# Kernel tuning notes

Measured on AMD Instinct MI355X. Metric: run time of the kernel, lower is better.

## Reference

```python
import jax, jax.numpy as jnp
import numpy as np

D_MODEL = 256
MLP_DIM = 1024
EPS = 1e-5

def _layernorm(x, g, b):
    mu = jnp.mean(x, axis=-1, keepdims=True)
    var = jnp.mean(jnp.square(x - mu), axis=-1, keepdims=True)
    return (x - mu) * jax.lax.rsqrt(var + EPS) * g + b

def setup_inputs() -> dict:
    key = jax.random.key(0)
    ks = jax.random.split(key, 4)
    d, m = D_MODEL, MLP_DIM
    x = jax.random.normal(ks[0], (8, 1024, 4, d), dtype=jnp.float32)
    w_qkv = jax.random.normal(ks[1], (3 * d, d), dtype=jnp.float32) * 0.05  # torch Linear weight (out,in)
    gamma1 = jnp.ones((d,), jnp.float32)
    beta1 = jnp.zeros((d,), jnp.float32)
    gamma2 = jnp.ones((d,), jnp.float32)
    beta2 = jnp.zeros((d,), jnp.float32)
    w1 = jax.random.normal(ks[2], (m, d), dtype=jnp.float32) * 0.05
    b1 = jnp.zeros((m,), jnp.float32)
    w2 = jax.random.normal(ks[3], (d, m), dtype=jnp.float32) * 0.05
    b2 = jnp.zeros((d,), jnp.float32)
    return {"x": x, "w_qkv": w_qkv, "gamma1": gamma1, "beta1": beta1,
            "gamma2": gamma2, "beta2": beta2, "w1": w1, "b1": b1, "w2": w2, "b2": b2}

def reference(x, w_qkv, gamma1, beta1, gamma2, beta2, w1, b1, w2, b2):
    bsz, n, h, d = x.shape
    scale = d ** -0.5
    # --- attention branch: x + attn(norm1(x)) ---
    xn = _layernorm(x, gamma1, beta1)
    # Linear(d, 3d): xn @ W^T, then reshape trailing 3d -> (d, 3) as in torch
    qkv = jnp.einsum('bnhd,ed->bnhe', xn, w_qkv).reshape(bsz, n * h, d, 3)
    q, k, v = qkv[..., 0], qkv[..., 1], qkv[..., 2]   # [b, n*h, d]
    dots = jnp.einsum('bid,bjd->bij', q, k) * scale   # [b, n*h, n*h]
    attn = jax.nn.softmax(dots, axis=-1)              # dropout=0 -> identity
    out = jnp.einsum('bij,bjd->bid', attn, v).reshape(bsz, n, h, d)
    x = x + out
    # --- mlp branch: x + mlp(norm2(x)) ---
    xn2 = _layernorm(x, gamma2, beta2)
    hid = jax.nn.silu(jnp.einsum('bnhd,md->bnhm', xn2, w1) + b1)
    x = x + jnp.einsum('bnhm,dm->bnhd', hid, w2) + b2
    return x
```

## Files before the change

### kernel.cpp

```cpp
#include <hip/hip_runtime.h>


typedef __attribute__((ext_vector_type(8))) short bf16x8;
typedef __attribute__((ext_vector_type(4))) short bf16x4;
typedef __attribute__((ext_vector_type(4))) float f32x4;
typedef __attribute__((ext_vector_type(16))) float f32x16;

static __device__ __forceinline__ short f2bf(float f) {
    union { float f; unsigned u; } v; v.f = f;
    unsigned r = (v.u + 0x7FFFu + ((v.u >> 16) & 1u)) >> 16;
    return (short)r;
}

static __device__ __forceinline__ void gll16(const void* g, void* l) {
    __builtin_amdgcn_global_load_lds(
        (const __attribute__((address_space(1))) unsigned*)g,
        (__attribute__((address_space(3))) unsigned*)l, 16, 0, 0);
}

__global__ __launch_bounds__(256) void k_cvt(const float* __restrict__ wqkv,
                                             const float* __restrict__ w1,
                                             const float* __restrict__ w2,
                                             short* __restrict__ owqkv,
                                             short* __restrict__ ow1,
                                             short* __restrict__ ow2) {
    int i = blockIdx.x * 256 + threadIdx.x;
    if (i < 196608) {
        int e = i >> 8, col = i & 255;
        int dd = e / 3, which = e - dd * 3;
        float v = wqkv[i];
        if (which == 0) v *= 0.0625f * 1.44269504f;
        owqkv[((which << 8) + dd) * 256 + col] = f2bf(v);
    }
    if (i < 262144) { ow1[i] = f2bf(w1[i]); ow2[i] = f2bf(w2[i]); }
}

__global__ __launch_bounds__(256) void k_ln(const float* __restrict__ x,
                                            const float* __restrict__ g,
                                            const float* __restrict__ bta,
                                            short* __restrict__ out) {
    int w = threadIdx.x >> 6, lane = threadIdx.x & 63;
    long row = (long)blockIdx.x * 4 + w;
    float4 v = *((const float4*)(x + row * 256) + lane);
    float s = v.x + v.y + v.z + v.w;
    float q = v.x * v.x + v.y * v.y + v.z * v.z + v.w * v.w;
    for (int off = 1; off < 64; off <<= 1) {
        s += __shfl_xor(s, off);
        q += __shfl_xor(q, off);
    }
    float mean = s * (1.0f / 256.0f);
    float var = q * (1.0f / 256.0f) - mean * mean;
    float rstd = rsqrtf(var + 1e-5f);
    float4 gg = *((const float4*)g + lane);
    float4 bb = *((const float4*)bta + lane);
    short4 o;
    o.x = f2bf((v.x - mean) * rstd * gg.x + bb.x);
    o.y = f2bf((v.y - mean) * rstd * gg.y + bb.y);
    o.z = f2bf((v.z - mean) * rstd * gg.z + bb.z);
    o.w = f2bf((v.w - mean) * rstd * gg.w + bb.w);
    *((short4*)(out + row * 256) + lane) = o;
}

__global__ __launch_bounds__(256) void k_qkv(const short* __restrict__ xn,
                                             const short* __restrict__ wb,
                                             short* __restrict__ Q,
                                             short* __restrict__ K,
                                             short* __restrict__ VT) {
    __shared__ __attribute__((aligned(16))) short lds_a[64 * 256];
    __shared__ __attribute__((aligned(16))) short lds_b[64 * 256];
    int t = threadIdx.x, w = t >> 6, l = t & 63, l5 = l & 31;
    int m0 = blockIdx.y * 64, n0 = blockIdx.x * 64;
    const char* ga = (const char*)xn + (long)m0 * 512;
    const char* gb = (const char*)wb + (long)n0 * 512;
    #pragma unroll
    for (int i = 0; i < 8; i++) {
        int r = w * 16 + i * 2 + (l >> 5);
        int off = r * 512 + ((l5 ^ (r & 31)) * 16);
        int ldst = (w * 16 + i * 2) * 512;
        gll16(ga + off, (char*)lds_a + ldst);
        gll16(gb + off, (char*)lds_b + ldst);
    }
    __syncthreads();
    int ln = l & 15, qd = l >> 4;
    int moff = (w >> 1) * 32, noff = (w & 1) * 32;
    f32x4 acc[2][2] = {};
    #pragma unroll
    for (int ks = 0; ks < 8; ks++) {
        int ca = ks * 4 + qd;
        int ra0 = moff + ln, ra1 = moff + 16 + ln;
        int rb0 = noff + ln, rb1 = noff + 16 + ln;
        bf16x8 a0 = *(const bf16x8*)((const char*)lds_a + ra0 * 512 + ((ca ^ (ra0 & 31)) * 16));
        bf16x8 a1 = *(const bf16x8*)((const char*)lds_a + ra1 * 512 + ((ca ^ (ra1 & 31)) * 16));
        bf16x8 b0 = *(const bf16x8*)((const char*)lds_b + rb0 * 512 + ((ca ^ (rb0 & 31)) * 16));
        bf16x8 b1 = *(const bf16x8*)((const char*)lds_b + rb1 * 512 + ((ca ^ (rb1 & 31)) * 16));
        acc[0][0] = __builtin_amdgcn_mfma_f32_16x16x32_bf16(a0, b0, acc[0][0], 0, 0, 0);
        acc[0][1] = __builtin_amdgcn_mfma_f32_16x16x32_bf16(a0, b1, acc[0][1], 0, 0, 0);
        acc[1][0] = __builtin_amdgcn_mfma_f32_16x16x32_bf16(a1, b0, acc[1][0], 0, 0, 0);
        acc[1][1] = __builtin_amdgcn_mfma_f32_16x16x32_bf16(a1, b1, acc[1][1], 0, 0, 0);
    }
    if (blockIdx.x < 8) {
        #pragma unroll
        for (int mi = 0; mi < 2; mi++)
            #pragma unroll
            for (int nj = 0; nj < 2; nj++)
                #pragma unroll
                for (int rg = 0; rg < 4; rg++) {
                    int gr = m0 + moff + mi * 16 + qd * 4 + rg;
                    int e = n0 + noff + nj * 16 + ln;
                    short bv = f2bf(acc[mi][nj][rg]);
                    if (e < 256) Q[(long)gr * 256 + e] = bv;
                    else K[(long)gr * 256 + (e - 256)] = bv;
                }
    } else {
        __syncthreads();
        short* scr = lds_a;
        #pragma unroll
        for (int mi = 0; mi < 2; mi++)
            #pragma unroll
            for (int nj = 0; nj < 2; nj++)
                #pragma unroll
                for (int rg = 0; rg < 4; rg++) {
                    int dl = noff + nj * 16 + ln;
                    int il = moff + mi * 16 + qd * 4 + rg;
                    scr[dl * 88 + il] = f2bf(acc[mi][nj][rg]);
                }
        __syncthreads();
        int bb = m0 >> 12, i0 = m0 & 4095;
        int dl = t >> 2, ch = t & 3;
        const int4* s4 = (const int4*)(scr + dl * 88 + ch * 16);
        int4 v0 = s4[0], v1 = s4[1];
        long vrow = ((long)(bb * 256 + (n0 - 512) + dl)) * 4096 + i0 + ch * 16;
        *(int4*)(VT + vrow) = v0;
        *(int4*)(VT + vrow + 8) = v1;
    }
}

__global__ __launch_bounds__(512, 2) void k_attn(const short* __restrict__ Q,
                                                 const short* __restrict__ K,
                                                 const short* __restrict__ VT,
                                                 const float* __restrict__ x,
                                                 float* __restrict__ out) {
    __shared__ __attribute__((aligned(16))) short lds_k[2][64 * 256];
    __shared__ __attribute__((aligned(16))) short lds_v[2][2][256 * 40];
    int t = threadIdx.x, w = t >> 6, l = t & 63, l5 = l & 31, h = l >> 5;
    int ww = w & 3, hkv = w >> 2;
    int b = blockIdx.x;
    int q0 = blockIdx.y * 128 + ww * 32;

    bf16x8 qf[16];
    {
        const short* qrow = Q + ((long)(b * 4096 + q0 + l5)) * 256;
        #pragma unroll
        for (int kc = 0; kc < 16; kc++) qf[kc] = *(const bf16x8*)(qrow + kc * 16 + h * 8);
    }
    f32x16 O[8] = {};
    float lsum = 0.f;

    const char* Kb = (const char*)(K + (long)b * 4096 * 256);
    const int4* gv = (const int4*)(VT + (long)b * 4096 * 256);

    int koff[4], klds[4];
    #pragma unroll
    for (int i = 0; i < 4; i++) {
        int r = w * 8 + i * 2 + (l >> 5);
        koff[i] = r * 512 + ((l5 ^ (r & 31)) * 16);
        klds[i] = (w * 8 + i * 2) * 512;
    }
    int vgbase[4], vloff[4];
    #pragma unroll
    for (int i = 0; i < 4; i++) {
        int c = t + 512 * i;
        int sub = c >> 10, cc = c & 1023, d = cc >> 2, ch = cc & 3;
        vgbase[i] = d * 512 + sub * 4 + ch;
        vloff[i] = sub * 20480 + d * 80 + ch * 16;
    }
    int4 vs[4];

    #pragma unroll
    for (int i = 0; i < 4; i++) vs[i] = gv[vgbase[i]];
    #pragma unroll
    for (int i = 0; i < 4; i++) gll16(Kb + koff[i], (char*)lds_k[0] + klds[i]);
    #pragma unroll
    for (int i = 0; i < 4; i++)
        *(int4*)((char*)lds_v + vloff[i]) = vs[i];
    __syncthreads();

    const char* lvmine = (const char*)lds_v + hkv * 20480;

    for (int jt = 0; jt < 64; jt++) {
        int cur = jt & 1;
        if (jt < 63) {
            #pragma unroll
            for (int i = 0; i < 4; i++) vs[i] = gv[vgbase[i] + (jt + 1) * 8];
            int ka = (jt + 1) * 32768;
            #pragma unroll
            for (int i = 0; i < 4; i++)
                gll16(Kb + ka + koff[i], (char*)lds_k[cur ^ 1] + klds[i]);
        }
        const short* lk = lds_k[cur] + hkv * 32 * 256;
        const char* lv = lvmine + cur * 40960;
        f32x16 st = {};
        #pragma unroll
        for (int kc = 0; kc < 16; kc++) {
            int cc = kc * 2 + h;
            bf16x8 a = *(const bf16x8*)(lk + (l5 * 32 + (cc ^ l5)) * 8);
            st = __builtin_amdgcn_mfma_f32_32x32x16_bf16(a, qf[kc], st, 0, 0, 0);
        }
        unsigned pw[4][2];
        #pragma unroll
        for (int r4 = 0; r4 < 4; r4++) {
            float p0 = __builtin_amdgcn_exp2f(st[r4 * 4 + 0]);
            float p1 = __builtin_amdgcn_exp2f(st[r4 * 4 + 1]);
            float p2 = __builtin_amdgcn_exp2f(st[r4 * 4 + 2]);
            float p3 = __builtin_amdgcn_exp2f(st[r4 * 4 + 3]);
            lsum += (p0 + p1) + (p2 + p3);
            union { float f; unsigned u; } u0, u1, u2, u3;
            u0.f = p0; u1.f = p1; u2.f = p2; u3.f = p3;
            pw[r4][0] = __builtin_amdgcn_perm(u1.u + 0x8000u, u0.u + 0x8000u, 0x07060302u);
            pw[r4][1] = __builtin_amdgcn_perm(u3.u + 0x8000u, u2.u + 0x8000u, 0x07060302u);
        }
        bf16x8 pfr[2];
        #pragma unroll
        for (int k2 = 0; k2 < 2; k2++) {
            unsigned a0 = pw[2 * k2][0], a1 = pw[2 * k2][1];
            unsigned b0 = pw[2 * k2 + 1][0], b1 = pw[2 * k2 + 1][1];
            asm("v_permlane32_swap_b32 %0, %1" : "+v"(a0), "+v"(b0));
            asm("v_permlane32_swap_b32 %0, %1" : "+v"(a1), "+v"(b1));
            union { unsigned u[4]; bf16x8 v; } f;
            f.u[0] = a0; f.u[1] = a1; f.u[2] = b0; f.u[3] = b1;
            pfr[k2] = f.v;
        }
        if (jt < 63) {
            #pragma unroll
            for (int i = 0; i < 4; i++)
                *(int4*)((char*)lds_v + (cur ^ 1) * 40960 + vloff[i]) = vs[i];
        }
        #pragma unroll
        for (int dt = 0; dt < 8; dt++) {
            const char* vbase = lv + (dt * 32 + l5) * 80;
            #pragma unroll
            for (int k2 = 0; k2 < 2; k2++) {
                bf16x8 va = *(const bf16x8*)(vbase + (k2 * 2 + h) * 16);
                O[dt] = __builtin_amdgcn_mfma_f32_32x32x16_bf16(va, pfr[k2], O[dt], 0, 0, 0);
            }
        }
        __syncthreads();
    }

    float lt = lsum + __shfl_xor(lsum, 32);
    float* lmrg = (float*)&lds_v[1][0][0];
    lmrg[hkv * 128 + ww * 32 + l5] = lt;
    __syncthreads();
    float ltot = lmrg[ww * 32 + l5] + lmrg[128 + ww * 32 + l5];
    float rinv = 1.0f / ltot;

    float* omrg = (float*)&lds_v[0][0][0];
    float* fscr = (float*)lds_k[0] + ww * (32 * 33);
    #pragma unroll
    for (int dt = 0; dt < 8; dt++) {
        if (hkv == 1) {
            #pragma unroll
            for (int r = 0; r < 16; r++) omrg[ww * 1024 + r * 64 + l] = O[dt][r];
        }
        __syncthreads();
        if (hkv == 0) {
            #pragma unroll
            for (int r = 0; r < 16; r++) {
                float Om = O[dt][r] + omrg[ww * 1024 + r * 64 + l];
                int drow = (r & 3) + 8 * (r >> 2) + 4 * h;
                fscr[drow * 33 + l5] = Om * rinv;
            }
            asm volatile("s_waitcnt lgkmcnt(0)" ::: "memory");
            #pragma unroll
            for (int it = 0; it < 16; it++) {
                int ql = it * 2 + h;
                float v = fscr[l5 * 33 + ql];
                long idx = ((long)(b * 4096 + q0 + ql)) * 256 + dt * 32 + l5;
                out[idx] = x[idx] + v;
            }
            asm volatile("s_waitcnt lgkmcnt(0)" ::: "memory");
        }
        __syncthreads();
    }
}

__global__ __launch_bounds__(512, 2) void k_mlp(const short* __restrict__ xn,
                                                const short* __restrict__ w1b,
                                                const short* __restrict__ w2b,
                                                const float* __restrict__ b1,
                                                const float* __restrict__ b2,
                                                float* __restrict__ out) {
    __shared__ __attribute__((aligned(16))) short lds_w[2][32 * 256];
    __shared__ __attribute__((aligned(16))) short lds_h[8][16 * 264];
    int t = threadIdx.x, w = t >> 6, l = t & 63, l5 = l & 31, ln = l & 15, qd = l >> 4;
    int R0 = blockIdx.x * 128 + w * 16;
    short* lhs = lds_h[w];

    bf16x8 a1f[8];
    #pragma unroll
    for (int kc = 0; kc < 8; kc++)
        a1f[kc] = *(const bf16x8*)(xn + (long)(R0 + ln) * 256 + kc * 32 + qd * 8);

    long s1off[2], s2off[2]; int wlds[2];
    #pragma unroll
    for (int i = 0; i < 2; i++) {
        int r = w * 4 + i * 2 + (l >> 5);
        int ch = l5 ^ (r & 31);
        s1off[i] = (long)r * 512 + ch * 16;
        s2off[i] = (long)r * 2048 + ch * 16;
        wlds[i] = (w * 4 + i * 2) * 512;
    }
    const char* W1c = (const char*)w1b;
    const char* W2c = (const char*)w2b;

    f32x4 Oc[8][2] = {};
    #pragma unroll
    for (int i = 0; i < 2; i++)
        gll16(W1c + s1off[i], (char*)lds_w[0] + wlds[i]);
    __syncthreads();
    int cur = 0;

    for (int pass = 0; pass < 4; pass++) {
        #pragma unroll
        for (int nt = 0; nt < 8; nt++) {
            if (nt < 7) {
                long base = (long)(pass * 256 + (nt + 1) * 32) * 512;
                #pragma unroll
                for (int i = 0; i < 2; i++)
                    gll16(W1c + base + s1off[i], (char*)lds_w[cur ^ 1] + wlds[i]);
            } else {
                long base = (long)pass * 512;
                #pragma unroll
                for (int i = 0; i < 2; i++)
                    gll16(W2c + base + s2off[i], (char*)lds_w[cur ^ 1] + wlds[i]);
            }
            const short* lw = lds_w[cur];
            #pragma unroll
            for (int g = 0; g < 2; g++) {
                int lr = g * 16 + ln;
                f32x4 acc = {};
                #pragma unroll
                for (int kc = 0; kc < 8; kc++) {
                    int cc = kc * 4 + qd;
                    bf16x8 bf = *(const bf16x8*)(lw + lr * 256 + (cc ^ lr) * 8);
                    acc = __builtin_amdgcn_mfma_f32_16x16x32_bf16(a1f[kc], bf, acc, 0, 0, 0);
                }
                float bb = b1[pass * 256 + nt * 32 + lr];
                #pragma unroll
                for (int rg = 0; rg < 4; rg++) {
                    float z = acc[rg] + bb;
                    float sv = z / (1.0f + __expf(-z));
                    lhs[(qd * 4 + rg) * 264 + nt * 32 + lr] = f2bf(sv);
                }
            }
            __syncthreads();
            cur ^= 1;
        }
        bf16x8 a2f[8];
        #pragma unroll
        for (int kc = 0; kc < 8; kc++)
            a2f[kc] = *(const bf16x8*)&lhs[ln * 264 + kc * 32 + qd * 8];
        #pragma unroll
        for (int nt = 0; nt < 8; nt++) {
            if (nt < 7) {
                long base = (long)((nt + 1) * 32) * 2048 + (long)pass * 512;
                #pragma unroll
                for (int i = 0; i < 2; i++)
                    gll16(W2c + base + s2off[i], (char*)lds_w[cur ^ 1] + wlds[i]);
            } else if (pass < 3) {
                long base = (long)((pass + 1) * 256) * 512;
                #pragma unroll
                for (int i = 0; i < 2; i++)
                    gll16(W1c + base + s1off[i], (char*)lds_w[cur ^ 1] + wlds[i]);
            }
            const short* lw = lds_w[cur];
            #pragma unroll
            for (int g = 0; g < 2; g++) {
                int lr = g * 16 + ln;
                #pragma unroll
                for (int kc = 0; kc < 8; kc++) {
                    int cc = kc * 4 + qd;
                    bf16x8 bf = *(const bf16x8*)(lw + lr * 256 + (cc ^ lr) * 8);
                    Oc[nt][g] = __builtin_amdgcn_mfma_f32_16x16x32_bf16(a2f[kc], bf, Oc[nt][g], 0, 0, 0);
                }
            }
            __syncthreads();
            cur ^= 1;
        }
    }
    #pragma unroll
    for (int nt = 0; nt < 8; nt++)
        #pragma unroll
        for (int g = 0; g < 2; g++) {
            int dd = nt * 32 + g * 16 + ln;
            float bb = b2[dd];
            #pragma unroll
            for (int rg = 0; rg < 4; rg++) {
                long idx = (long)(R0 + qd * 4 + rg) * 256 + dd;
                out[idx] = out[idx] + Oc[nt][g][rg] + bb;
            }
        }
}

extern "C" void kernel_launch(void* const* d_in, const int* in_sizes, int n_in,
                              void* d_out, int out_size, void* d_ws, size_t ws_size,
                              hipStream_t stream) {
    const float* x    = (const float*)d_in[0];
    const float* wqkv = (const float*)d_in[1];
    const float* g1   = (const float*)d_in[2];
    const float* be1  = (const float*)d_in[3];
    const float* g2   = (const float*)d_in[4];
    const float* be2  = (const float*)d_in[5];
    const float* w1   = (const float*)d_in[6];
    const float* b1   = (const float*)d_in[7];
    const float* w2   = (const float*)d_in[8];
    const float* b2   = (const float*)d_in[9];
    float* out = (float*)d_out;
    char* ws = (char*)d_ws;
    short* WQKV = (short*)(ws);
    short* W1B  = (short*)(ws + (512l << 10));
    short* W2B  = (short*)(ws + (1l << 20));
    short* XN   = (short*)(ws + (2l << 20));
    short* Qb   = (short*)(ws + (18l << 20));
    short* Kb   = (short*)(ws + (34l << 20));
    short* VTb  = (short*)(ws + (50l << 20));

    k_cvt<<<1024, 256, 0, stream>>>(wqkv, w1, w2, WQKV, W1B, W2B);
    k_ln<<<8192, 256, 0, stream>>>(x, g1, be1, XN);
    k_qkv<<<dim3(12, 512), 256, 0, stream>>>(XN, WQKV, Qb, Kb, VTb);
    k_attn<<<dim3(8, 32), 512, 0, stream>>>(Qb, Kb, VTb, x, out);
    k_ln<<<8192, 256, 0, stream>>>(out, g2, be2, XN);
    k_mlp<<<256, 512, 0, stream>>>(XN, W1B, W2B, b1, b2, out);
}
```

Measured before the change: 410.1 us.

## Restructure QKV GEMM to stream weight tiles per row block; halve MLP block size

The QKV projection now launches one 512-thread block per 128-row tile. Each block keeps its activation fragments in registers and loops over all 12 output column tiles, double-buffering the weight tiles in LDS via global_load_lds. This replaces the old 12x512 grid that reloaded the A tile for every column tile, cutting activation traffic and block count but adding a serial loop and barriers per tile. The MLP kernel moves to 256-thread blocks of 64 rows with twice as many blocks, each thread loading more of the weight tile, to raise block-level parallelism at the cost of more total weight reloads.

```diff
diff --git a/kernel.cpp b/kernel.cpp
--- a/kernel.cpp
+++ b/kernel.cpp
@@ -61,77 +61,93 @@
     *((short4*)(out + row * 256) + lane) = o;
 }
 
-__global__ __launch_bounds__(256) void k_qkv(const short* __restrict__ xn,
-                                             const short* __restrict__ wb,
-                                             short* __restrict__ Q,
-                                             short* __restrict__ K,
-                                             short* __restrict__ VT) {
-    __shared__ __attribute__((aligned(16))) short lds_a[64 * 256];
-    __shared__ __attribute__((aligned(16))) short lds_b[64 * 256];
+__global__ __launch_bounds__(512, 2) void k_qkv(const short* __restrict__ xn,
+                                                const short* __restrict__ wb,
+                                                short* __restrict__ Q,
+                                                short* __restrict__ K,
+                                                short* __restrict__ VT) {
+    __shared__ __attribute__((aligned(16))) short lds_b[2][64 * 256];
+    __shared__ __attribute__((aligned(16))) short lds_t[64 * 136];
     int t = threadIdx.x, w = t >> 6, l = t & 63, l5 = l & 31;
-    int m0 = blockIdx.y * 64, n0 = blockIdx.x * 64;
-    const char* ga = (const char*)xn + (long)m0 * 512;
-    const char* gb = (const char*)wb + (long)n0 * 512;
-    #pragma unroll
-    for (int i = 0; i < 8; i++) {
-        int r = w * 16 + i * 2 + (l >> 5);
-        int off = r * 512 + ((l5 ^ (r & 31)) * 16);
-        int ldst = (w * 16 + i * 2) * 512;
-        gll16(ga + off, (char*)lds_a + ldst);
-        gll16(gb + off, (char*)lds_b + ldst);
-    }
+    int ln = l & 15, qd = l >> 4;
+    int m0 = blockIdx.x * 128;
+    int moff = (w >> 1) * 32, noff = (w & 1) * 32;
+
+    bf16x8 af[2][8];
+    #pragma unroll
+    for (int mi = 0; mi < 2; mi++)
+        #pragma unroll
+        for (int kc = 0; kc < 8; kc++)
+            af[mi][kc] = *(const bf16x8*)(xn + (long)(m0 + moff + mi * 16 + ln) * 256 + kc * 32 + qd * 8);
+
+    int boff[4], blds[4];
+    #pragma unroll
+    for (int i = 0; i < 4; i++) {
+        int r = w * 8 + i * 2 + (l >> 5);
+        boff[i] = r * 512 + ((l5 ^ (r & 31)) * 16);
+        blds[i] = (w * 8 + i * 2) * 512;
+    }
+    const char* gB = (const char*)wb;
+    #pragma unroll
+    for (int i = 0; i < 4; i++) gll16(gB + boff[i], (char*)lds_b[0] + blds[i]);
     __syncthreads();
-    int ln = l & 15, qd = l >> 4;
-    int moff = (w >> 1) * 32, noff = (w & 1) * 32;
-    f32x4 acc[2][2] = {};
-    #pragma unroll
-    for (int ks = 0; ks < 8; ks++) {
-        int ca = ks * 4 + qd;
-        int ra0 = moff + ln, ra1 = moff + 16 + ln;
-        int rb0 = noff + ln, rb1 = noff + 16 + ln;
-        bf16x8 a0 = *(const bf16x8*)((const char*)lds_a + ra0 * 512 + ((ca ^ (ra0 & 31)) * 16));
-        bf16x8 a1 = *(const bf16x8*)((const char*)lds_a + ra1 * 512 + ((ca ^ (ra1 & 31)) * 16));
-        bf16x8 b0 = *(const bf16x8*)((const char*)lds_b + rb0 * 512 + ((ca ^ (rb0 & 31)) * 16));
-        bf16x8 b1 = *(const bf16x8*)((const char*)lds_b + rb1 * 512 + ((ca ^ (rb1 & 31)) * 16));
-        acc[0][0] = __builtin_amdgcn_mfma_f32_16x16x32_bf16(a0, b0, acc[0][0], 0, 0, 0);
-        acc[0][1] = __builtin_amdgcn_mfma_f32_16x16x32_bf16(a0, b1, acc[0][1], 0, 0, 0);
-        acc[1][0] = __builtin_amdgcn_mfma_f32_16x16x32_bf16(a1, b0, acc[1][0], 0, 0, 0);
-        acc[1][1] = __builtin_amdgcn_mfma_f32_16x16x32_bf16(a1, b1, acc[1][1], 0, 0, 0);
-    }
-    if (blockIdx.x < 8) {
-        #pragma unroll
-        for (int mi = 0; mi < 2; mi++)
-            #pragma unroll
-            for (int nj = 0; nj < 2; nj++)
-                #pragma unroll
-                for (int rg = 0; rg < 4; rg++) {
-                    int gr = m0 + moff + mi * 16 + qd * 4 + rg;
-                    int e = n0 + noff + nj * 16 + ln;
-                    short bv = f2bf(acc[mi][nj][rg]);
-                    if (e < 256) Q[(long)gr * 256 + e] = bv;
-                    else K[(long)gr * 256 + (e - 256)] = bv;
-                }
-    } else {
+
+    for (int nt = 0; nt < 12; nt++) {
+        int cur = nt & 1;
+        if (nt < 11) {
+            long base = (long)(nt + 1) * 32768;
+            #pragma unroll
+            for (int i = 0; i < 4; i++)
+                gll16(gB + base + boff[i], (char*)lds_b[cur ^ 1] + blds[i]);
+        }
+        const char* lb = (const char*)lds_b[cur];
+        f32x4 acc[2][2] = {};
+        #pragma unroll
+        for (int ks = 0; ks < 8; ks++) {
+            int ca = ks * 4 + qd;
+            int rb0 = noff + ln, rb1 = noff + 16 + ln;
+            bf16x8 b0 = *(const bf16x8*)(lb + rb0 * 512 + ((ca ^ (rb0 & 31)) * 16));
+            bf16x8 b1 = *(const bf16x8*)(lb + rb1 * 512 + ((ca ^ (rb1 & 31)) * 16));
+            acc[0][0] = __builtin_amdgcn_mfma_f32_16x16x32_bf16(af[0][ks], b0, acc[0][0], 0, 0, 0);
+            acc[0][1] = __builtin_amdgcn_mfma_f32_16x16x32_bf16(af[0][ks], b1, acc[0][1], 0, 0, 0);
+            acc[1][0] = __builtin_amdgcn_mfma_f32_16x16x32_bf16(af[1][ks], b0, acc[1][0], 0, 0, 0);
+            acc[1][1] = __builtin_amdgcn_mfma_f32_16x16x32_bf16(af[1][ks], b1, acc[1][1], 0, 0, 0);
+        }
+        int e0 = nt * 64;
+        if (e0 < 512) {
+            #pragma unroll
+            for (int mi = 0; mi < 2; mi++)
+                #pragma unroll
+                for (int nj = 0; nj < 2; nj++)
+                    #pragma unroll
+                    for (int rg = 0; rg < 4; rg++) {
+                        int gr = m0 + moff + mi * 16 + qd * 4 + rg;
+                        int e = e0 + noff + nj * 16 + ln;
+                        short bv = f2bf(acc[mi][nj][rg]);
+                        if (e < 256) Q[(long)gr * 256 + e] = bv;
+                        else K[(long)gr * 256 + (e - 256)] = bv;
+                    }
+        } else {
+            #pragma unroll
+            for (int mi = 0; mi < 2; mi++)
+                #pragma unroll
+                for (int nj = 0; nj < 2; nj++)
+                    #pragma unroll
+                    for (int rg = 0; rg < 4; rg++) {
+                        int dl = noff + nj * 16 + ln;
+                        int il = moff + mi * 16 + qd * 4 + rg;
+                        lds_t[dl * 136 + il] = f2bf(acc[mi][nj][rg]);
+                    }
+            __syncthreads();
+            int bb = m0 >> 12, i0 = m0 & 4095;
+            int dl = t >> 3, ch = t & 7;
+            const int4* s4 = (const int4*)(lds_t + dl * 136 + ch * 16);
+            int4 v0 = s4[0], v1 = s4[1];
+            long vrow = ((long)(bb * 256 + (e0 - 512) + dl)) * 4096 + i0 + ch * 16;
+            *(int4*)(VT + vrow) = v0;
+            *(int4*)(VT + vrow + 8) = v1;
+        }
         __syncthreads();
-        short* scr = lds_a;
-        #pragma unroll
-        for (int mi = 0; mi < 2; mi++)
-            #pragma unroll
-            for (int nj = 0; nj < 2; nj++)
-                #pragma unroll
-                for (int rg = 0; rg < 4; rg++) {
-                    int dl = noff + nj * 16 + ln;
-                    int il = moff + mi * 16 + qd * 4 + rg;
-                    scr[dl * 88 + il] = f2bf(acc[mi][nj][rg]);
-                }
-        __syncthreads();
-        int bb = m0 >> 12, i0 = m0 & 4095;
-        int dl = t >> 2, ch = t & 3;
-        const int4* s4 = (const int4*)(scr + dl * 88 + ch * 16);
-        int4 v0 = s4[0], v1 = s4[1];
-        long vrow = ((long)(bb * 256 + (n0 - 512) + dl)) * 4096 + i0 + ch * 16;
-        *(int4*)(VT + vrow) = v0;
-        *(int4*)(VT + vrow + 8) = v1;
     }
 }
 
@@ -284,16 +300,16 @@
     }
 }
 
-__global__ __launch_bounds__(512, 2) void k_mlp(const short* __restrict__ xn,
-                                                const short* __restrict__ w1b,
-                                                const short* __restrict__ w2b,
-                                                const float* __restrict__ b1,
-                                                const float* __restrict__ b2,
-                                                float* __restrict__ out) {
+__global__ __launch_bounds__(256) void k_mlp(const short* __restrict__ xn,
+                                             const short* __restrict__ w1b,
+                                             const short* __restrict__ w2b,
+                                             const float* __restrict__ b1,
+                                             const float* __restrict__ b2,
+                                             float* __restrict__ out) {
     __shared__ __attribute__((aligned(16))) short lds_w[2][32 * 256];
-    __shared__ __attribute__((aligned(16))) short lds_h[8][16 * 264];
+    __shared__ __attribute__((aligned(16))) short lds_h[4][16 * 264];
     int t = threadIdx.x, w = t >> 6, l = t & 63, l5 = l & 31, ln = l & 15, qd = l >> 4;
-    int R0 = blockIdx.x * 128 + w * 16;
+    int R0 = blockIdx.x * 64 + w * 16;
     short* lhs = lds_h[w];
 
     bf16x8 a1f[8];
@@ -301,21 +317,21 @@
     for (int kc = 0; kc < 8; kc++)
         a1f[kc] = *(const bf16x8*)(xn + (long)(R0 + ln) * 256 + kc * 32 + qd * 8);
 
-    long s1off[2], s2off[2]; int wlds[2];
-    #pragma unroll
-    for (int i = 0; i < 2; i++) {
-        int r = w * 4 + i * 2 + (l >> 5);
+    long s1off[4], s2off[4]; int wlds[4];
+    #pragma unroll
+    for (int i = 0; i < 4; i++) {
+        int r = w * 8 + i * 2 + (l >> 5);
         int ch = l5 ^ (r & 31);
         s1off[i] = (long)r * 512 + ch * 16;
         s2off[i] = (long)r * 2048 + ch * 16;
-        wlds[i] = (w * 4 + i * 2) * 512;
+        wlds[i] = (w * 8 + i * 2) * 512;
     }
     const char* W1c = (const char*)w1b;
     const char* W2c = (const char*)w2b;
 
     f32x4 Oc[8][2] = {};
     #pragma unroll
-    for (int i = 0; i < 2; i++)
+    for (int i = 0; i < 4; i++)
         gll16(W1c + s1off[i], (char*)lds_w[0] + wlds[i]);
     __syncthreads();
     int cur = 0;
@@ -326,12 +342,12 @@
             if (nt < 7) {
                 long base = (long)(pass * 256 + (nt + 1) * 32) * 512;
                 #pragma unroll
-                for (int i = 0; i < 2; i++)
+                for (int i = 0; i < 4; i++)
                     gll16(W1c + base + s1off[i], (char*)lds_w[cur ^ 1] + wlds[i]);
             } else {
                 long base = (long)pass * 512;
                 #pragma unroll
-                for (int i = 0; i < 2; i++)
+                for (int i = 0; i < 4; i++)
                     gll16(W2c + base + s2off[i], (char*)lds_w[cur ^ 1] + wlds[i]);
             }
             const short* lw = lds_w[cur];
@@ -365,12 +381,12 @@
             if (nt < 7) {
                 long base = (long)((nt + 1) * 32) * 2048 + (long)pass * 512;
                 #pragma unroll
-                for (int i = 0; i < 2; i++)
+                for (int i = 0; i < 4; i++)
                     gll16(W2c + base + s2off[i], (char*)lds_w[cur ^ 1] + wlds[i]);
             } else if (pass < 3) {
                 long base = (long)((pass + 1) * 256) * 512;
                 #pragma unroll
-                for (int i = 0; i < 2; i++)
+                for (int i = 0; i < 4; i++)
                     gll16(W1c + base + s1off[i], (char*)lds_w[cur ^ 1] + wlds[i]);
             }
             const short* lw = lds_w[cur];
@@ -427,8 +443,8 @@
 
     k_cvt<<<1024, 256, 0, stream>>>(wqkv, w1, w2, WQKV, W1B, W2B);
     k_ln<<<8192, 256, 0, stream>>>(x, g1, be1, XN);
-    k_qkv<<<dim3(12, 512), 256, 0, stream>>>(XN, WQKV, Qb, Kb, VTb);
+    k_qkv<<<256, 512, 0, stream>>>(XN, WQKV, Qb, Kb, VTb);
     k_attn<<<dim3(8, 32), 512, 0, stream>>>(Qb, Kb, VTb, x, out);
     k_ln<<<8192, 256, 0, stream>>>(out, g2, be2, XN);
-    k_mlp<<<256, 512, 0, stream>>>(XN, W1B, W2B, b1, b2, out);
-}
+    k_mlp<<<512, 256, 0, stream>>>(XN, W1B, W2B, b1, b2, out);
+}
```

Result: faster. 388.8 us (median of 2 runs) (-5.2%).
